# Kernel tuning notes

Hardware: AMD Instinct MI355X
Metric: run time of the kernel (lower is better)

## Reference

```python
import jax, jax.numpy as jnp
import numpy as np

BATCH, SEQ_LEN, EMBED_DIM = 32, 2048, 128
N_QLAYERS = 2
N_WIRES = 18  # ceil(log2(128*2048)) ; 2**18 == 128*2048 exactly


def rot_matrices(p):
    # p: [n_wires, 3] (phi, theta, omega) -> [n_wires, 2, 2] complex64
    # PennyLane/torchquantum Rot convention: RZ(omega) RY(theta) RZ(phi)
    phi, th, om = p[..., 0], p[..., 1], p[..., 2]
    c, s = jnp.cos(th / 2), jnp.sin(th / 2)
    e = lambda a: jnp.exp(1j * a)  # float32 -> complex64 (weak complex scalar)
    m00 = e(-(phi + om) / 2) * c
    m01 = -e((phi - om) / 2) * s
    m10 = e(-(phi - om) / 2) * s
    m11 = e((phi + om) / 2) * c
    return jnp.stack([jnp.stack([m00, m01], -1), jnp.stack([m10, m11], -1)], -2)


def apply_1q(state, U, w):
    # state: [B, 2^n] complex; wire 0 is the most-significant qubit axis
    B = state.shape[0]
    L, R = 2 ** w, 2 ** (N_WIRES - 1 - w)
    s = state.reshape(B, L, 2, R)
    s = jnp.einsum('ij,bljr->blir', U, s)
    return s.reshape(B, -1)


def apply_cnot(state, c, t):
    # flip target bit t where control bit c == 1
    B = state.shape[0]
    s = state.reshape((B,) + (2,) * N_WIRES)
    ca, ta = c + 1, t + 1
    s0 = jnp.take(s, 0, axis=ca)
    s1 = jnp.take(s, 1, axis=ca)
    flip_axis = ta - 1 if ta > ca else ta  # target axis index after removing control axis
    s1 = jnp.flip(s1, axis=flip_axis)
    return jnp.stack([s0, s1], axis=ca).reshape(B, -1)


def setup_inputs() -> dict:
    key = jax.random.key(0)
    k1, k2 = jax.random.split(key)
    x = jax.random.normal(k1, (BATCH, SEQ_LEN, EMBED_DIM), dtype=jnp.float32)
    params = jax.random.uniform(k2, (N_QLAYERS, N_WIRES, 3), dtype=jnp.float32,
                                minval=-np.pi, maxval=np.pi)
    return {"x": x, "params": params}


def reference(x, params):
    B = x.shape[0]
    v = x.reshape(B, -1)
    # StateEncoder: L2-normalize amplitudes (2^N_WIRES == SEQ_LEN*EMBED_DIM, no padding needed)
    v = v / jnp.sqrt(jnp.sum(v * v, axis=-1, keepdims=True))
    state = v.astype(jnp.complex64)
    for l in range(N_QLAYERS):
        U = rot_matrices(params[l])  # [N_WIRES, 2, 2]
        for w in range(N_WIRES):
            state = apply_1q(state, U[w], w)
        for i in range(N_WIRES):
            state = apply_cnot(state, (i + l) % N_WIRES, (i + l + 1) % N_WIRES)
    return jnp.abs(state).reshape(B, SEQ_LEN, EMBED_DIM)
```

## Files before the change

### kernel.cpp

```cpp
#include <hip/hip_runtime.h>
#include <hip/hip_fp16.h>

#define NW 18
#define NSTATE (1u << NW)
#define NBATCH 32
#define TOTAL (NBATCH * (size_t)NSTATE)

typedef float v2f __attribute__((ext_vector_type(2)));
typedef _Float16 h2v __attribute__((ext_vector_type(2)));

struct Masks { unsigned m[18]; };

__device__ __forceinline__ v2f pk_mulsw(v2f g, v2f b) {
    v2f d;
    asm("v_pk_mul_f32 %0, %1, %2 op_sel:[1,1] op_sel_hi:[1,0] neg_lo:[1,0]"
        : "=v"(d) : "v"(g), "v"(b));
    return d;
}
__device__ __forceinline__ v2f pk_fmare(v2f g, v2f a, v2f c) {
    v2f d;
    asm("v_pk_fma_f32 %0, %1, %2, %3 op_sel:[0,0,0] op_sel_hi:[0,1,1]"
        : "=v"(d) : "v"(g), "v"(a), "v"(c));
    return d;
}
__device__ __forceinline__ v2f pk_fmasw(v2f g, v2f a, v2f c) {
    v2f d;
    asm("v_pk_fma_f32 %0, %1, %2, %3 op_sel:[1,1,0] op_sel_hi:[1,0,1] neg_lo:[1,0,0]"
        : "=v"(d) : "v"(g), "v"(a), "v"(c));
    return d;
}
__device__ __forceinline__ v2f cmul(v2f g, v2f x) { return pk_fmare(g, x, pk_mulsw(g, x)); }
__device__ __forceinline__ v2f cmad(v2f g, v2f x, v2f c) { return pk_fmare(g, x, pk_fmasw(g, x, c)); }

__device__ __forceinline__ void bfly(v2f& a, v2f& b, v2f g00, v2f g01, v2f g10, v2f g11) {
    v2f na = cmad(g00, a, cmul(g01, b));
    v2f nb = cmad(g10, a, cmul(g11, b));
    a = na; b = nb;
}

__device__ __forceinline__ unsigned pack(v2f v) {
    return __builtin_bit_cast(unsigned, __builtin_amdgcn_cvt_pkrtz(v.x, v.y));
}
__device__ __forceinline__ v2f unpack(unsigned u) {
    h2v h = __builtin_bit_cast(h2v, u);
    return (v2f){(float)h.x, (float)h.y};
}

__device__ __forceinline__ int swz(int n) { return n ^ ((n >> 5) & 31); }

__device__ __forceinline__ constexpr int ctzc(int x) {
    int c = 0; while (!(x & 1)) { x >>= 1; c++; } return c;
}

#define GATES(gb)                                                      \
    const float4 G0_ = Ut[(17-(gb))*2+0], G1_ = Ut[(17-(gb))*2+1];     \
    const v2f g00 = {G0_.x, G0_.y}, g01 = {G0_.z, G0_.w};              \
    const v2f g10 = {G1_.x, G1_.y}, g11 = {G1_.z, G1_.w};

__global__ void prep(const float* __restrict__ params, float4* __restrict__ Utab) {
    int i = threadIdx.x;
    if (i < 36) {
        float phi = params[i*3+0], th = params[i*3+1], om = params[i*3+2];
        float ch = cosf(th*0.5f), sh = sinf(th*0.5f);
        float a0 = -0.5f*(phi+om);
        float a1 =  0.5f*(phi-om);
        float c0 = cosf(a0), s0 = sinf(a0);
        float c1 = cosf(a1), s1 = sinf(a1);
        Utab[i*2+0] = make_float4(c0*ch,  s0*ch, -c1*sh, -s1*sh);
        Utab[i*2+1] = make_float4(c1*sh, -s1*sh,  c0*ch, -s0*ch);
    }
}

__global__ __launch_bounds__(256) void normk(const float* __restrict__ x,
                                             float* __restrict__ partials) {
    int t = threadIdx.x;
    size_t base = (size_t)blockIdx.x * 4096;
    const float4* p = (const float4*)(x + base);
    float s = 0.f;
#pragma unroll
    for (int j = 0; j < 4; j++) {
        float4 q = p[t + j*256];
        s += q.x*q.x + q.y*q.y + q.z*q.z + q.w*q.w;
    }
#pragma unroll
    for (int m = 32; m >= 1; m >>= 1) s += __shfl_xor(s, m, 64);
    __shared__ float ws[4];
    if ((t & 63) == 0) ws[t >> 6] = s;
    __syncthreads();
    if (t == 0) partials[blockIdx.x] = ws[0]+ws[1]+ws[2]+ws[3];
}

template<int SRC_F32>
__global__ __launch_bounds__(256, 4) void passA(const void* __restrict__ src,
                                                unsigned* __restrict__ dst,
                                                const float4* __restrict__ Utab,
                                                int layer) {
    __shared__ unsigned sm[4096];
    const int t = threadIdx.x;
    const size_t base = (size_t)blockIdx.x * 4096;
    v2f v[16];

    if (SRC_F32) {
        const float4* xs = (const float4*)((const float*)src + base + (size_t)t * 16);
#pragma unroll
        for (int j = 0; j < 4; j++) {
            float4 q = xs[j];
            v[j*4+0] = (v2f){q.x, 0.f};
            v[j*4+1] = (v2f){q.y, 0.f};
            v[j*4+2] = (v2f){q.z, 0.f};
            v[j*4+3] = (v2f){q.w, 0.f};
        }
    } else {
        const uint4* xs = (const uint4*)((const unsigned*)src + base + (size_t)t * 16);
#pragma unroll
        for (int j = 0; j < 4; j++) {
            uint4 q = xs[j];
            v[j*4+0] = unpack(q.x);
            v[j*4+1] = unpack(q.y);
            v[j*4+2] = unpack(q.z);
            v[j*4+3] = unpack(q.w);
        }
    }

    const float4* Ut = Utab + (size_t)layer * 36;

#pragma unroll
    for (int b = 0; b < 4; b++) {
        GATES(b);
#pragma unroll
        for (int k = 0; k < 16; k++)
            if (!(k & (1 << b))) bfly(v[k], v[k | (1 << b)], g00, g01, g10, g11);
    }

#pragma unroll
    for (int k = 0; k < 16; k++)
        sm[swz((t << 4) | k)] = pack(v[k]);
    __syncthreads();
#pragma unroll
    for (int k = 0; k < 16; k++)
        v[k] = unpack(sm[swz((t & 15) | (k << 4) | ((t >> 4) << 8))]);

#pragma unroll
    for (int b = 4; b < 8; b++) {
        GATES(b);
        const int pb = 1 << (b - 4);
#pragma unroll
        for (int k = 0; k < 16; k++)
            if (!(k & pb)) bfly(v[k], v[k | pb], g00, g01, g10, g11);
    }

#pragma unroll
    for (int k = 0; k < 16; k++)
        sm[swz((t & 15) | (k << 4) | ((t >> 4) << 8))] = pack(v[k]);
    __syncthreads();
#pragma unroll
    for (int k = 0; k < 16; k++)
        v[k] = unpack(sm[swz(t | (k << 8))]);

#pragma unroll
    for (int b = 8; b < 12; b++) {
        GATES(b);
        const int pb = 1 << (b - 8);
#pragma unroll
        for (int k = 0; k < 16; k++)
            if (!(k & pb)) bfly(v[k], v[k | pb], g00, g01, g10, g11);
    }

#pragma unroll
    for (int k = 0; k < 16; k++)
        dst[base + (t | (k << 8))] = pack(v[k]);
}

template<int LAST>
__global__ __launch_bounds__(256, 4) void passB(const unsigned* __restrict__ src,
                                                void* __restrict__ dst,
                                                const float4* __restrict__ Utab,
                                                const float* __restrict__ partials,
                                                int layer, Masks mk) {
    __shared__ unsigned sm[4096];
    const int t = threadIdx.x;
    const unsigned blk = blockIdx.x;
    const unsigned batch = blk >> 6;
    const unsigned chunk = blk & 63;
    const unsigned low = chunk * 64 + (t & 63);
    const unsigned j = t >> 6;
    const size_t bb = (size_t)batch << NW;

    v2f v[16];
#pragma unroll
    for (int k = 0; k < 16; k++) {
        unsigned h = (j << 4) | k;
        v[k] = unpack(src[bb + ((size_t)h << 12) + low]);
    }

    const float4* Ut = Utab + (size_t)layer * 36;
#pragma unroll
    for (int b = 12; b < 16; b++) {
        GATES(b);
        const int pb = 1 << (b - 12);
#pragma unroll
        for (int k = 0; k < 16; k++)
            if (!(k & pb)) bfly(v[k], v[k | pb], g00, g01, g10, g11);
    }

#pragma unroll
    for (int k = 0; k < 16; k++) {
        unsigned h = (j << 4) | k;
        sm[(h << 6) | (t & 63)] = pack(v[k]);
    }
    __syncthreads();
#pragma unroll
    for (int q = 0; q < 4; q++)
#pragma unroll
        for (int r = 0; r < 4; r++) {
            unsigned h = (q << 4) | (j << 2) | r;
            v[(q << 2) | r] = unpack(sm[(h << 6) | (t & 63)]);
        }

    {
        GATES(16);
#pragma unroll
        for (int k = 0; k < 16; k++)
            if (!(k & 4)) bfly(v[k], v[k | 4], g00, g01, g10, g11);
    }
    {
        GATES(17);
#pragma unroll
        for (int k = 0; k < 16; k++)
            if (!(k & 8)) bfly(v[k], v[k | 8], g00, g01, g10, g11);
    }

    unsigned f = 0;
#pragma unroll
    for (int kk = 0; kk < 12; kk++) f ^= ((low >> kk) & 1u) ? mk.m[kk] : 0u;
    if (j & 1) f ^= mk.m[14];
    if (j & 2) f ^= mk.m[15];

    float sc = 1.f;
    if (LAST) {
        float nrm = 0.f;
#pragma unroll
        for (int i = 0; i < 64; i++) nrm += partials[batch * 64 + i];
        sc = rsqrtf(nrm);
    }

    const unsigned gm0 = mk.m[12], gm1 = mk.m[13], gm2 = mk.m[16], gm3 = mk.m[17];
    unsigned fs = f;
#pragma unroll
    for (int i = 0; i < 16; i++) {
        if (i) {
            const int c = ctzc(i);
            fs ^= (c == 0) ? gm0 : (c == 1) ? gm1 : (c == 2) ? gm2 : gm3;
        }
        const int s = i ^ (i >> 1);
        if (LAST) {
            ((float*)dst)[bb + fs] = sc * sqrtf(fmaf(v[s].x, v[s].x, v[s].y*v[s].y));
        } else {
            ((unsigned*)dst)[bb + fs] = pack(v[s]);
        }
    }
}

static void chain_masks(int l, Masks* mk) {
    unsigned rows[18];
    for (int j = 0; j < 18; j++) rows[j] = 1u << j;
    for (int i = 0; i < 18; i++) {
        int cw = (i + l) % 18, tw = (i + l + 1) % 18;
        rows[17 - tw] ^= rows[17 - cw];
    }
    for (int k = 0; k < 18; k++) {
        unsigned cm = 0;
        for (int j = 0; j < 18; j++) cm |= ((rows[j] >> k) & 1u) << j;
        mk->m[k] = cm;
    }
}

extern "C" void kernel_launch(void* const* d_in, const int* in_sizes, int n_in,
                              void* d_out, int out_size, void* d_ws, size_t ws_size,
                              hipStream_t stream) {
    const float* x      = (const float*)d_in[0];
    const float* params = (const float*)d_in[1];

    char* ws = (char*)d_ws;
    unsigned* bufA  = (unsigned*)ws;
    unsigned* bufB  = (unsigned*)(ws + TOTAL * 4);
    float4*   Utab  = (float4*)(ws + TOTAL * 8);
    float* partials = (float*)(ws + TOTAL * 8 + 4096);

    Masks mk1, mk2;
    chain_masks(0, &mk1);
    chain_masks(1, &mk2);

    prep<<<1, 64, 0, stream>>>(params, Utab);
    normk<<<2048, 256, 0, stream>>>(x, partials);
    passA<1><<<2048, 256, 0, stream>>>((const void*)x, bufA, Utab, 0);
    passB<0><<<2048, 256, 0, stream>>>(bufA, (void*)bufB, Utab, partials, 0, mk1);
    passA<0><<<2048, 256, 0, stream>>>((const void*)bufB, bufB, Utab, 1);
    passB<1><<<2048, 256, 0, stream>>>(bufB, d_out, Utab, partials, 1, mk2);
}
```

Baseline: 158.5 us.

## Fuse gate prep and norm reduction into first passA, raise occupancy bound

Removes the separate prep and normk kernels. The first passA now builds the gate matrices per block in shared memory, with block 0 also writing the global table, and computes the per-block sum of squares from the x values it already loads. This drops two launches and a full extra read of x. It also raises launch_bounds min-blocks from 4 to 8 on passA and passB, which may force register limits and cause spills; every block now also recomputes the trig for the gates.

```diff
diff --git a/kernel.cpp b/kernel.cpp
--- a/kernel.cpp
+++ b/kernel.cpp
@@ -57,59 +57,59 @@
     const v2f g00 = {G0_.x, G0_.y}, g01 = {G0_.z, G0_.w};              \
     const v2f g10 = {G1_.x, G1_.y}, g11 = {G1_.z, G1_.w};
 
-__global__ void prep(const float* __restrict__ params, float4* __restrict__ Utab) {
-    int i = threadIdx.x;
-    if (i < 36) {
-        float phi = params[i*3+0], th = params[i*3+1], om = params[i*3+2];
-        float ch = cosf(th*0.5f), sh = sinf(th*0.5f);
-        float a0 = -0.5f*(phi+om);
-        float a1 =  0.5f*(phi-om);
-        float c0 = cosf(a0), s0 = sinf(a0);
-        float c1 = cosf(a1), s1 = sinf(a1);
-        Utab[i*2+0] = make_float4(c0*ch,  s0*ch, -c1*sh, -s1*sh);
-        Utab[i*2+1] = make_float4(c1*sh, -s1*sh,  c0*ch, -s0*ch);
-    }
-}
-
-__global__ __launch_bounds__(256) void normk(const float* __restrict__ x,
-                                             float* __restrict__ partials) {
-    int t = threadIdx.x;
-    size_t base = (size_t)blockIdx.x * 4096;
-    const float4* p = (const float4*)(x + base);
-    float s = 0.f;
-#pragma unroll
-    for (int j = 0; j < 4; j++) {
-        float4 q = p[t + j*256];
-        s += q.x*q.x + q.y*q.y + q.z*q.z + q.w*q.w;
-    }
-#pragma unroll
-    for (int m = 32; m >= 1; m >>= 1) s += __shfl_xor(s, m, 64);
-    __shared__ float ws[4];
-    if ((t & 63) == 0) ws[t >> 6] = s;
-    __syncthreads();
-    if (t == 0) partials[blockIdx.x] = ws[0]+ws[1]+ws[2]+ws[3];
-}
-
-template<int SRC_F32>
-__global__ __launch_bounds__(256, 4) void passA(const void* __restrict__ src,
+__device__ __forceinline__ void make_gate(const float* __restrict__ p,
+                                          float4& G0, float4& G1) {
+    float phi = p[0], th = p[1], om = p[2];
+    float ch = cosf(th*0.5f), sh = sinf(th*0.5f);
+    float a0 = -0.5f*(phi+om), a1 = 0.5f*(phi-om);
+    float c0 = cosf(a0), s0 = sinf(a0);
+    float c1 = cosf(a1), s1 = sinf(a1);
+    G0 = make_float4(c0*ch,  s0*ch, -c1*sh, -s1*sh);
+    G1 = make_float4(c1*sh, -s1*sh,  c0*ch, -s0*ch);
+}
+
+template<int FIRST>
+__global__ __launch_bounds__(256, 8) void passA(const void* __restrict__ src,
                                                 unsigned* __restrict__ dst,
-                                                const float4* __restrict__ Utab,
+                                                float4* __restrict__ Utab,
+                                                float* __restrict__ partials,
+                                                const float* __restrict__ params,
                                                 int layer) {
     __shared__ unsigned sm[4096];
+    __shared__ float4 gl[72];
+    __shared__ float wsum[4];
     const int t = threadIdx.x;
     const size_t base = (size_t)blockIdx.x * 4096;
     v2f v[16];
-
-    if (SRC_F32) {
+    const float4* Ut;
+    float ss = 0.f;
+
+    if (FIRST) {
         const float4* xs = (const float4*)((const float*)src + base + (size_t)t * 16);
+        float4 q[4];
+#pragma unroll
+        for (int j = 0; j < 4; j++) q[j] = xs[j];
+
+        if (t < 36) {
+            float4 G0, G1;
+            make_gate(params + t*3, G0, G1);
+            gl[t*2] = G0; gl[t*2+1] = G1;
+            if (blockIdx.x == 0) { Utab[t*2] = G0; Utab[t*2+1] = G1; }
+        }
+
 #pragma unroll
         for (int j = 0; j < 4; j++) {
-            float4 q = xs[j];
-            v[j*4+0] = (v2f){q.x, 0.f};
-            v[j*4+1] = (v2f){q.y, 0.f};
-            v[j*4+2] = (v2f){q.z, 0.f};
-            v[j*4+3] = (v2f){q.w, 0.f};
-        }
+            v[j*4+0] = (v2f){q[j].x, 0.f};
+            v[j*4+1] = (v2f){q[j].y, 0.f};
+            v[j*4+2] = (v2f){q[j].z, 0.f};
+            v[j*4+3] = (v2f){q[j].w, 0.f};
+            ss += q[j].x*q[j].x + q[j].y*q[j].y + q[j].z*q[j].z + q[j].w*q[j].w;
+        }
+#pragma unroll
+        for (int m = 32; m >= 1; m >>= 1) ss += __shfl_xor(ss, m, 64);
+        if ((t & 63) == 0) wsum[t >> 6] = ss;
+        __syncthreads();
+        Ut = gl;
     } else {
         const uint4* xs = (const uint4*)((const unsigned*)src + base + (size_t)t * 16);
 #pragma unroll
@@ -120,9 +120,8 @@
             v[j*4+2] = unpack(q.z);
             v[j*4+3] = unpack(q.w);
         }
-    }
-
-    const float4* Ut = Utab + (size_t)layer * 36;
+        Ut = (const float4*)Utab + (size_t)layer * 36;
+    }
 
 #pragma unroll
     for (int b = 0; b < 4; b++) {
@@ -136,6 +135,8 @@
     for (int k = 0; k < 16; k++)
         sm[swz((t << 4) | k)] = pack(v[k]);
     __syncthreads();
+    if (FIRST && t == 0)
+        partials[blockIdx.x] = wsum[0] + wsum[1] + wsum[2] + wsum[3];
 #pragma unroll
     for (int k = 0; k < 16; k++)
         v[k] = unpack(sm[swz((t & 15) | (k << 4) | ((t >> 4) << 8))]);
@@ -172,7 +173,7 @@
 }
 
 template<int LAST>
-__global__ __launch_bounds__(256, 4) void passB(const unsigned* __restrict__ src,
+__global__ __launch_bounds__(256, 8) void passB(const unsigned* __restrict__ src,
                                                 void* __restrict__ dst,
                                                 const float4* __restrict__ Utab,
                                                 const float* __restrict__ partials,
@@ -291,10 +292,8 @@
     chain_masks(0, &mk1);
     chain_masks(1, &mk2);
 
-    prep<<<1, 64, 0, stream>>>(params, Utab);
-    normk<<<2048, 256, 0, stream>>>(x, partials);
-    passA<1><<<2048, 256, 0, stream>>>((const void*)x, bufA, Utab, 0);
+    passA<1><<<2048, 256, 0, stream>>>((const void*)x, bufA, Utab, partials, params, 0);
     passB<0><<<2048, 256, 0, stream>>>(bufA, (void*)bufB, Utab, partials, 0, mk1);
-    passA<0><<<2048, 256, 0, stream>>>((const void*)bufB, bufB, Utab, 1);
+    passA<0><<<2048, 256, 0, stream>>>((const void*)bufB, bufB, Utab, partials, params, 1);
     passB<1><<<2048, 256, 0, stream>>>(bufB, d_out, Utab, partials, 1, mk2);
 }
```

Measured after the change: 168.3 us. +6.2%, slower.
